# Optimization experiments

Hardware: AMD Instinct MI355X
Metric: run time of the kernel (lower is better)

The kernel has to match this reference:

```python
import jax, jax.numpy as jnp
import numpy as np

DIM = 2048
RANK = 8
SCALE_INIT = 0.01
N_TOKENS = 8192


def setup_inputs() -> dict:
    key = jax.random.key(0)
    kx, ku, kv = jax.random.split(key, 3)
    x = jax.random.normal(kx, (N_TOKENS, DIM), dtype=jnp.float32)
    U = jax.random.normal(ku, (DIM, RANK), dtype=jnp.float32) * SCALE_INIT
    V = jax.random.normal(kv, (DIM, RANK), dtype=jnp.float32) * SCALE_INIT
    gate = jnp.float32(-2.0)
    return {"x": x, "U": U, "V": V, "gate": gate}


def reference(x, U, V, gate):
    # omega = (U V^T - V U^T) * sigmoid(gate)  -- skew-symmetric generator
    UV = U @ V.T                               # [dim, dim]
    omega = (UV - UV.T) * jax.nn.sigmoid(gate)
    I = jnp.eye(x.shape[-1], dtype=x.dtype)
    half = omega * 0.5
    # Cayley transform: R = (I - omega/2)^{-1} (I + omega/2)
    R = jnp.linalg.solve(I - half, I + half)   # [dim, dim]
    return x @ R.T
```

## Files before the change

### kernel.cpp

```cpp
#include <hip/hip_runtime.h>
#include <hip/hip_fp16.h>
#include <cstddef>

#define DIM 2048
#define NTOK 8192
#define NEUMANN_ITERS 6


typedef _Float16 h4 __attribute__((ext_vector_type(4)));
typedef float f32x4 __attribute__((ext_vector_type(4)));

__device__ __forceinline__ unsigned pkh(float lo, float hi) {
  auto p = __builtin_amdgcn_cvt_pkrtz(lo, hi);
  return __builtin_bit_cast(unsigned, p);
}

__global__ __launch_bounds__(256) void rora_gram(
    const float* __restrict__ U, const float* __restrict__ V,
    float* __restrict__ prod) {
  const int e = blockIdx.x;
  const int q = e >> 6;
  const int i = (e >> 3) & 7, j = e & 7;
  const float* A = (q == 2) ? V : U;
  const float* B = (q == 0) ? U : V;
  const int t = threadIdx.x;
  float acc = 0.f;
#pragma unroll
  for (int s = 0; s < 8; ++s) {
    const int d = s * 256 + t;
    acc = fmaf(A[d * 8 + i], B[d * 8 + j], acc);
  }
#pragma unroll
  for (int m = 1; m < 64; m <<= 1) acc += __shfl_xor(acc, m, 64);
  __shared__ float wsum[4];
  if ((t & 63) == 0) wsum[t >> 6] = acc;
  __syncthreads();
  if (t == 0) prod[e] = (wsum[0] + wsum[1]) + (wsum[2] + wsum[3]);
}

__global__ __launch_bounds__(256) void rora_fused(
    const float* __restrict__ x, const float* __restrict__ U,
    const float* __restrict__ V, const float* __restrict__ gate,
    const float* __restrict__ prod, float* __restrict__ out) {
  __shared__ uint4 uvQ[4][DIM / 2];
  __shared__ float prodS[192];
  __shared__ float Gs[16][17];
  __shared__ float Bm[16][17];
  __shared__ float Ya[16][17];
  __shared__ float Yb[16][17];
  __shared__ float Ared[4][64][4];
  __shared__ float As[16][17];
  const int t = threadIdx.x;
  const int lane = t & 63, wv = t >> 6;

  {
    const float4* U4 = (const float4*)U;
    const float4* V4 = (const float4*)V;
#pragma unroll
    for (int rep = 0; rep < 4; ++rep) {
      const int P = rep * 256 + t;
      const float4 a0 = U4[4 * P + 0], a1 = U4[4 * P + 1];
      const float4 a2 = U4[4 * P + 2], a3 = U4[4 * P + 3];
      const float4 b0 = V4[4 * P + 0], b1 = V4[4 * P + 1];
      const float4 b2 = V4[4 * P + 2], b3 = V4[4 * P + 3];
      uvQ[0][P] = make_uint4(pkh(a0.x, a2.x), pkh(a0.y, a2.y),
                             pkh(a0.z, a2.z), pkh(a0.w, a2.w));
      uvQ[1][P] = make_uint4(pkh(a1.x, a3.x), pkh(a1.y, a3.y),
                             pkh(a1.z, a3.z), pkh(a1.w, a3.w));
      uvQ[2][P] = make_uint4(pkh(b0.x, b2.x), pkh(b0.y, b2.y),
                             pkh(b0.z, b2.z), pkh(b0.w, b2.w));
      uvQ[3][P] = make_uint4(pkh(b1.x, b3.x), pkh(b1.y, b3.y),
                             pkh(b1.z, b3.z), pkh(b1.w, b3.w));
    }
  }

  if (t < 192) prodS[t] = prod[t];
  __syncthreads();
  const float sg = 1.f / (1.f + expf(-gate[0]));
  {
    const int r = t >> 4, c = t & 15;
    float g;
    if (r < 8) g = (c < 8) ? sg * prodS[64 + c * 8 + r]
                           : sg * prodS[128 + r * 8 + (c - 8)];
    else       g = (c < 8) ? -sg * prodS[(r - 8) * 8 + c]
                           : -sg * prodS[64 + (r - 8) * 8 + (c - 8)];
    const float b = ((r == c) ? 1.f : 0.f) + 0.5f * g;
    Gs[r][c] = g;
    Bm[r][c] = b;
    Ya[r][c] = b;
  }
  __syncthreads();
#pragma unroll
  for (int m = 0; m < NEUMANN_ITERS; ++m) {
    const int r = t >> 4, c = t & 15;
    const float (*Yp)[17] = (m & 1) ? Yb : Ya;
    float (*Yn)[17] = (m & 1) ? Ya : Yb;
    float acc = Bm[r][c];
#pragma unroll
    for (int j = 0; j < 16; ++j)
      acc = fmaf(0.5f * Gs[r][j], Yp[j][c], acc);
    Yn[r][c] = acc;
    __syncthreads();
  }

  const int row0 = blockIdx.x * 16;
  const int rA = lane & 15, g = lane >> 4;
  f32x4 acc = {0.f, 0.f, 0.f, 0.f};
  {
    const float* xrow = x + (size_t)(row0 + rA) * DIM;
    const int q1 = rA >> 2, c1 = rA & 3;
    const unsigned* uvW = (const unsigned*)&uvQ[q1][0];
#pragma unroll 4
    for (int step = 0; step < 32; ++step) {
      const int d0 = wv * 512 + step * 16 + g * 4;
      const float4 xv = *(const float4*)(xrow + d0);
      uint2 au = {pkh(xv.x, xv.y), pkh(xv.z, xv.w)};
      const h4 af = __builtin_bit_cast(h4, au);
      const int P0 = d0 >> 1;
      uint2 bu = {uvW[P0 * 4 + c1], uvW[(P0 + 1) * 4 + c1]};
      const h4 bf = __builtin_bit_cast(h4, bu);
      acc = __builtin_amdgcn_mfma_f32_16x16x16f16(af, bf, acc, 0, 0, 0);
    }
  }
  Ared[wv][lane][0] = acc[0];
  Ared[wv][lane][1] = acc[1];
  Ared[wv][lane][2] = acc[2];
  Ared[wv][lane][3] = acc[3];
  __syncthreads();
  {
    const int l = t & 63, j = t >> 6;
    const float s = (Ared[0][l][j] + Ared[1][l][j]) +
                    (Ared[2][l][j] + Ared[3][l][j]);
    As[(l >> 4) * 4 + j][l & 15] = s;
  }
  __syncthreads();

  h4 cf;
  {
    const float hs = 0.5f * sg;
    const int r = rA;
    float cj[4];
#pragma unroll
    for (int j = 0; j < 4; ++j) {
      const int k = g * 4 + j;
      float s = 0.f;
#pragma unroll
      for (int jj = 0; jj < 8; ++jj) {
        const float zA = Ya[k][jj] + ((k == jj) ? 1.f : 0.f);
        const float zB = Ya[k][8 + jj] + ((k == 8 + jj) ? 1.f : 0.f);
        s = fmaf(zA, As[r][8 + jj], s);
        s = fmaf(-zB, As[r][jj], s);
      }
      cj[j] = hs * s;
    }
    uint2 cu = {pkh(cj[0], cj[1]), pkh(cj[2], cj[3])};
    cf = __builtin_bit_cast(h4, cu);
  }

  {
    const int par = rA & 1;
    for (int nt = wv * 32; nt < wv * 32 + 32; ++nt) {
      const int dcol0 = nt * 16;
      const uint4 wq = uvQ[g][(dcol0 + rA) >> 1];
      const unsigned w01 = par ? ((wq.x >> 16) | (wq.y & 0xffff0000u))
                               : ((wq.x & 0xffffu) | (wq.y << 16));
      const unsigned w23 = par ? ((wq.z >> 16) | (wq.w & 0xffff0000u))
                               : ((wq.z & 0xffffu) | (wq.w << 16));
      uint2 bu = {w01, w23};
      const h4 bf = __builtin_bit_cast(h4, bu);
      f32x4 z4 = {0.f, 0.f, 0.f, 0.f};
      const f32x4 o = __builtin_amdgcn_mfma_f32_16x16x16f16(cf, bf, z4, 0, 0, 0);
      const float* xp = x + (size_t)(row0 + g * 4) * DIM + dcol0 + rA;
      float* op = out + (size_t)(row0 + g * 4) * DIM + dcol0 + rA;
#pragma unroll
      for (int j = 0; j < 4; ++j)
        op[(size_t)j * DIM] = xp[(size_t)j * DIM] + o[j];
    }
  }
}

extern "C" void kernel_launch(void* const* d_in, const int* in_sizes, int n_in,
                              void* d_out, int out_size, void* d_ws, size_t ws_size,
                              hipStream_t stream) {
  const float* x    = (const float*)d_in[0];
  const float* U    = (const float*)d_in[1];
  const float* V    = (const float*)d_in[2];
  const float* gate = (const float*)d_in[3];
  float* out = (float*)d_out;
  float* prodw = (float*)d_ws;

  rora_gram<<<192, 256, 0, stream>>>(U, V, prodw);
  rora_fused<<<NTOK / 16, 256, 0, stream>>>(x, U, V, gate, prodw, out);
}
```

Baseline: 46.47 us.

## Fuse Gram matrix computation into main kernel via MFMA on staged U/V

Removes the separate rora_gram launch and has every block compute the 16x16 Gram matrix W^T W of [U V] from the fp16 copy already staged in shared memory, using MFMA with per-wave partial sums reduced through LDS. This eliminates one kernel launch and the global workspace round trip. In exchange each block redoes the Gram computation redundantly, which adds one extra sync and reduction stage, and the Gram is now computed in fp16 inputs instead of fp32. The shared plane is also padded by one element, and the Bm buffer is replaced by recomputing I + G/2 on the fly.

```diff
diff --git a/kernel.cpp b/kernel.cpp
--- a/kernel.cpp
+++ b/kernel.cpp
@@ -5,6 +5,7 @@
 #define DIM 2048
 #define NTOK 8192
 #define NEUMANN_ITERS 6
+#define PLANE (DIM / 2 + 1)
 
 
 typedef _Float16 h4 __attribute__((ext_vector_type(4)));
@@ -15,43 +16,20 @@
   return __builtin_bit_cast(unsigned, p);
 }
 
-__global__ __launch_bounds__(256) void rora_gram(
-    const float* __restrict__ U, const float* __restrict__ V,
-    float* __restrict__ prod) {
-  const int e = blockIdx.x;
-  const int q = e >> 6;
-  const int i = (e >> 3) & 7, j = e & 7;
-  const float* A = (q == 2) ? V : U;
-  const float* B = (q == 0) ? U : V;
-  const int t = threadIdx.x;
-  float acc = 0.f;
-#pragma unroll
-  for (int s = 0; s < 8; ++s) {
-    const int d = s * 256 + t;
-    acc = fmaf(A[d * 8 + i], B[d * 8 + j], acc);
-  }
-#pragma unroll
-  for (int m = 1; m < 64; m <<= 1) acc += __shfl_xor(acc, m, 64);
-  __shared__ float wsum[4];
-  if ((t & 63) == 0) wsum[t >> 6] = acc;
-  __syncthreads();
-  if (t == 0) prod[e] = (wsum[0] + wsum[1]) + (wsum[2] + wsum[3]);
-}
-
 __global__ __launch_bounds__(256) void rora_fused(
     const float* __restrict__ x, const float* __restrict__ U,
     const float* __restrict__ V, const float* __restrict__ gate,
-    const float* __restrict__ prod, float* __restrict__ out) {
-  __shared__ uint4 uvQ[4][DIM / 2];
-  __shared__ float prodS[192];
+    float* __restrict__ out) {
+  __shared__ uint4 uvQ[4][PLANE];
   __shared__ float Gs[16][17];
-  __shared__ float Bm[16][17];
   __shared__ float Ya[16][17];
   __shared__ float Yb[16][17];
+  __shared__ float Wtw[16][17];
   __shared__ float Ared[4][64][4];
   __shared__ float As[16][17];
   const int t = threadIdx.x;
   const int lane = t & 63, wv = t >> 6;
+  const int rA = lane & 15, g = lane >> 4;
 
   {
     const float4* U4 = (const float4*)U;
@@ -73,21 +51,40 @@
                              pkh(b1.z, b3.z), pkh(b1.w, b3.w));
     }
   }
+  __syncthreads();
 
-  if (t < 192) prodS[t] = prod[t];
+  {
+    const int q1 = rA >> 2, c1 = rA & 3;
+    const unsigned* uvW = (const unsigned*)&uvQ[q1][0];
+    f32x4 acc = {0.f, 0.f, 0.f, 0.f};
+#pragma unroll 4
+    for (int step = 0; step < 32; ++step) {
+      const int d0 = wv * 512 + step * 16 + g * 4;
+      const int P0 = d0 >> 1;
+      uint2 bu = {uvW[P0 * 4 + c1], uvW[(P0 + 1) * 4 + c1]};
+      const h4 wf = __builtin_bit_cast(h4, bu);
+      acc = __builtin_amdgcn_mfma_f32_16x16x16f16(wf, wf, acc, 0, 0, 0);
+    }
+    Ared[wv][lane][0] = acc[0];
+    Ared[wv][lane][1] = acc[1];
+    Ared[wv][lane][2] = acc[2];
+    Ared[wv][lane][3] = acc[3];
+  }
   __syncthreads();
+  {
+    const int l = t & 63, j = t >> 6;
+    const float s = (Ared[0][l][j] + Ared[1][l][j]) +
+                    (Ared[2][l][j] + Ared[3][l][j]);
+    Wtw[(l >> 4) * 4 + j][l & 15] = s;
+  }
+  __syncthreads();
+
   const float sg = 1.f / (1.f + expf(-gate[0]));
   {
     const int r = t >> 4, c = t & 15;
-    float g;
-    if (r < 8) g = (c < 8) ? sg * prodS[64 + c * 8 + r]
-                           : sg * prodS[128 + r * 8 + (c - 8)];
-    else       g = (c < 8) ? -sg * prodS[(r - 8) * 8 + c]
-                           : -sg * prodS[64 + (r - 8) * 8 + (c - 8)];
-    const float b = ((r == c) ? 1.f : 0.f) + 0.5f * g;
-    Gs[r][c] = g;
-    Bm[r][c] = b;
-    Ya[r][c] = b;
+    const float gv = (r < 8) ? sg * Wtw[r + 8][c] : -sg * Wtw[r - 8][c];
+    Gs[r][c] = gv;
+    Ya[r][c] = ((r == c) ? 1.f : 0.f) + 0.5f * gv;
   }
   __syncthreads();
 #pragma unroll
@@ -95,7 +92,7 @@
     const int r = t >> 4, c = t & 15;
     const float (*Yp)[17] = (m & 1) ? Yb : Ya;
     float (*Yn)[17] = (m & 1) ? Ya : Yb;
-    float acc = Bm[r][c];
+    float acc = ((r == c) ? 1.f : 0.f) + 0.5f * Gs[r][c];
 #pragma unroll
     for (int j = 0; j < 16; ++j)
       acc = fmaf(0.5f * Gs[r][j], Yp[j][c], acc);
@@ -104,7 +101,6 @@
   }
 
   const int row0 = blockIdx.x * 16;
-  const int rA = lane & 15, g = lane >> 4;
   f32x4 acc = {0.f, 0.f, 0.f, 0.f};
   {
     const float* xrow = x + (size_t)(row0 + rA) * DIM;
@@ -187,8 +183,6 @@
   const float* V    = (const float*)d_in[2];
   const float* gate = (const float*)d_in[3];
   float* out = (float*)d_out;
-  float* prodw = (float*)d_ws;
 
-  rora_gram<<<192, 256, 0, stream>>>(U, V, prodw);
-  rora_fused<<<NTOK / 16, 256, 0, stream>>>(x, U, V, gate, prodw, out);
+  rora_fused<<<NTOK / 16, 256, 0, stream>>>(x, U, V, gate, out);
 }
```

After: 43.00 us. 7.5% less time.
